# Kernel tuning notes

Measured on AMD Instinct MI355X. Metric: run time of the kernel, lower is better.

Reference implementation:

```python
import jax, jax.numpy as jnp
import numpy as np

H, N, N_SSM, CHANNELS, SEQ_L = 1024, 64, 1024, 1, 2048


def setup_inputs() -> dict:
    key = jax.random.key(0)
    ks = jax.random.split(key, 7)
    log_dt = jax.random.uniform(ks[0], (H,), jnp.float32,
                                minval=np.log(1e-3).astype(np.float32),
                                maxval=np.log(1e-1).astype(np.float32))
    return {
        "L": SEQ_L,
        "log_dt": log_dt,
        "C_re": jax.random.normal(ks[1], (CHANNELS, H, N), jnp.float32),
        "C_im": jax.random.normal(ks[2], (CHANNELS, H, N), jnp.float32),
        "B_re": jax.random.normal(ks[3], (N_SSM, N), jnp.float32),
        "B_im": jax.random.normal(ks[4], (N_SSM, N), jnp.float32),
        "inv_A_real": jax.random.normal(ks[5], (N_SSM, N), jnp.float32),
        "A_imag": jax.random.normal(ks[6], (N_SSM, N), jnp.float32),
    }


def reference(L, log_dt, C_re, C_im, B_re, B_im, inv_A_real, A_imag):
    dt = jnp.exp(log_dt)                                  # (H,)
    C = C_re + 1j * C_im                                  # (channels, H, N)
    A = -jnp.exp(inv_A_real) + 1j * A_imag                # (n_ssm, N)
    B = B_re + 1j * B_im                                  # (n_ssm, N)
    rep = log_dt.shape[0] // A.shape[0]                   # H // n_ssm
    A = jnp.tile(A, (rep, 1))                             # 't n -> (v t) n'
    B = jnp.tile(B, (rep, 1))[None]                       # (1, H, N)
    dtA = A * dt[:, None]                                 # (H, N)
    # C <- (B * C) scaled by bilinear-discretization factor dt / (1 - dtA/2)
    Cm = (B[:, None, :, :] * C).reshape(-1, dt.shape[0], A.shape[-1])  # (channels, H, N)
    Cm = Cm * (dt[:, None] / (1.0 - dtA / 2))             # (channels, H, N)
    # log_vandermonde: K = 2 * Re[ sum_n Cm * exp(dtA * l) ]  -> (channels, H, L)
    l = jnp.arange(L, dtype=jnp.float32)
    vand = jnp.exp(dtA[:, :, None] * l)                   # (H, N, L) complex
    K = 2.0 * jnp.einsum('chn,hnl->chl', Cm, vand).real   # (channels, H, L)
    return K
```

## Files before the change

kernel.cpp:

```cpp
#include <hip/hip_runtime.h>


typedef __attribute__((ext_vector_type(8))) _Float16 f16x8;
typedef __attribute__((ext_vector_type(2))) __fp16   h16x2;
typedef __attribute__((ext_vector_type(4))) float    f32x4;

#define Hdim 1024
#define Ndim 64
#define Ldim 2048
#define KPAD 136
#define CPAD 36

#define LOG2E  1.4426950408889634f
#define INV2PI 0.15915494309189535f

__device__ __forceinline__ void cmul(float& xr, float& xi, float yr, float yi) {
    const float tr = fmaf(xr, yr, -(xi * yi));
    xi = fmaf(xr, yi, xi * yr);
    xr = tr;
}

__device__ __forceinline__ void expz(float ar2, float airev, float t,
                                     float& zr, float& zi) {
    const float e = __builtin_amdgcn_exp2f(ar2 * t);
    float f = airev * t;
    f -= floorf(f);
    zr = e * __builtin_amdgcn_cosf(f);
    zi = e * __builtin_amdgcn_sinf(f);
}

__global__ __launch_bounds__(512, 8) void icmf_mfma(
    const float* __restrict__ log_dt,
    const float* __restrict__ C_re, const float* __restrict__ C_im,
    const float* __restrict__ B_re, const float* __restrict__ B_im,
    const float* __restrict__ inv_A_real, const float* __restrict__ A_imag,
    float* __restrict__ out)
{
    __shared__ __align__(16) _Float16 sA[64][KPAD];
    __shared__ __align__(16) _Float16 sB[32][KPAD];
    __shared__ __align__(16) float    sC[64][CPAD];

    const int h   = blockIdx.x;
    const int tid = threadIdx.x;
    const int w   = tid >> 6;
    const int n   = tid & 63;

    {
        const int idx = h * Ndim + n;
        const float dt = __builtin_amdgcn_exp2f(log_dt[h] * LOG2E);
        const float ar = -dt * __builtin_amdgcn_exp2f(inv_A_real[idx] * LOG2E);
        const float ai =  dt * A_imag[idx];
        const float dre = 1.0f - 0.5f * ar;
        const float dim = -0.5f * ai;
        const float kk  = dt / (dre * dre + dim * dim);
        const float sre =  dre * kk;
        const float sim = -dim * kk;
        const float br = B_re[idx], bi = B_im[idx];
        const float cr = C_re[idx], ci = C_im[idx];
        const float bcr = br * cr - bi * ci;
        const float bci = br * ci + bi * cr;
        const float cmr = 2.0f * (bcr * sre - bci * sim);
        const float cmi = 2.0f * (bcr * sim + bci * sre);
        const float ar2   = ar * LOG2E;
        const float airev = ai * INV2PI;

        float z1r, z1i, z32r, z32i, vr, vi, tr_, ti_;
        expz(ar2, airev, 1.0f,              z1r,  z1i);
        expz(ar2, airev, 32.0f,             z32r, z32i);
        expz(ar2, airev, (float)(4 * w),    vr,   vi);
        expz(ar2, airev, (float)(256 * w),  tr_,  ti_);
        float ur = fmaf(cmr, tr_, -(cmi * ti_));
        float ui = fmaf(cmr, ti_,   cmi * tr_);

#pragma unroll
        for (int s = 0; s < 8; ++s) {
            *(h16x2*)&sA[8 * w + s][2 * n] = __builtin_amdgcn_cvt_pkrtz(ur, -ui);
            cmul(ur, ui, z32r, z32i);
        }
#pragma unroll
        for (int s = 0; s < 4; ++s) {
            *(h16x2*)&sB[4 * w + s][2 * n] = __builtin_amdgcn_cvt_pkrtz(vr, vi);
            cmul(vr, vi, z1r, z1i);
        }
    }
    __syncthreads();

    const int mt   = w >> 1;
    const int nt   = w & 1;
    const int mrow = n & 15;
    const int kgrp = n >> 4;
    f32x4 acc = {0.f, 0.f, 0.f, 0.f};
#pragma unroll
    for (int ks = 0; ks < 4; ++ks) {
        const int k0 = ks * 32 + kgrp * 8;
        const f16x8 af = *(const f16x8*)&sA[16 * mt + mrow][k0];
        const f16x8 bf = *(const f16x8*)&sB[16 * nt + mrow][k0];
        acc = __builtin_amdgcn_mfma_f32_16x16x32_f16(af, bf, acc, 0, 0, 0);
    }

#pragma unroll
    for (int r = 0; r < 4; ++r)
        sC[16 * mt + kgrp * 4 + r][16 * nt + mrow] = acc[r];
    __syncthreads();

    {
        const f32x4 v = *(const f32x4*)&sC[tid >> 3][(tid & 7) * 4];
        *(f32x4*)(out + h * Ldim + tid * 4) = v;
    }
}

extern "C" void kernel_launch(void* const* d_in, const int* in_sizes, int n_in,
                              void* d_out, int out_size, void* d_ws, size_t ws_size,
                              hipStream_t stream) {
    const float* log_dt     = (const float*)d_in[1];
    const float* C_re       = (const float*)d_in[2];
    const float* C_im       = (const float*)d_in[3];
    const float* B_re       = (const float*)d_in[4];
    const float* B_im       = (const float*)d_in[5];
    const float* inv_A_real = (const float*)d_in[6];
    const float* A_imag     = (const float*)d_in[7];
    float* out = (float*)d_out;

    icmf_mfma<<<Hdim, 512, 0, stream>>>(log_dt, C_re, C_im, B_re, B_im,
                                        inv_A_real, A_imag, out);
}
```

Before: 10.54 us.

## Split each head into eight single-wave blocks, dropping barriers and LDS staging

Each head's 64x32 output tile is now computed by eight independent 64-thread blocks instead of one 512-thread block, so no __syncthreads is needed and results go straight from the MFMA accumulator to global memory instead of through an LDS transpose. The cost is redundant work: every block recomputes the per-n discretization parameters and four complex exponentials, and builds 16 rows each of A and B instead of 8 and 4. The direct stores are 64-byte row segments rather than fully coalesced float4 writes, and the launch bounds and block count change to match.

```diff
diff --git a/kernel.cpp b/kernel.cpp
--- a/kernel.cpp
+++ b/kernel.cpp
@@ -9,7 +9,6 @@
 #define Ndim 64
 #define Ldim 2048
 #define KPAD 136
-#define CPAD 36
 
 #define LOG2E  1.4426950408889634f
 #define INV2PI 0.15915494309189535f
@@ -29,21 +28,22 @@
     zi = e * __builtin_amdgcn_sinf(f);
 }
 
-__global__ __launch_bounds__(512, 8) void icmf_mfma(
+__global__ __launch_bounds__(64, 4) void icmf_mfma(
     const float* __restrict__ log_dt,
     const float* __restrict__ C_re, const float* __restrict__ C_im,
     const float* __restrict__ B_re, const float* __restrict__ B_im,
     const float* __restrict__ inv_A_real, const float* __restrict__ A_imag,
     float* __restrict__ out)
 {
-    __shared__ __align__(16) _Float16 sA[64][KPAD];
-    __shared__ __align__(16) _Float16 sB[32][KPAD];
-    __shared__ __align__(16) float    sC[64][CPAD];
+    __shared__ __align__(16) _Float16 sA[16][KPAD];
+    __shared__ __align__(16) _Float16 sB[16][KPAD];
 
-    const int h   = blockIdx.x;
-    const int tid = threadIdx.x;
-    const int w   = tid >> 6;
-    const int n   = tid & 63;
+    const int bid  = blockIdx.x;
+    const int h    = bid >> 3;
+    const int tile = bid & 7;
+    const int mt   = tile >> 1;
+    const int nt   = tile & 1;
+    const int n    = threadIdx.x;
 
     {
         const int idx = h * Ndim + n;
@@ -65,48 +65,40 @@
         const float airev = ai * INV2PI;
 
         float z1r, z1i, z32r, z32i, vr, vi, tr_, ti_;
-        expz(ar2, airev, 1.0f,              z1r,  z1i);
-        expz(ar2, airev, 32.0f,             z32r, z32i);
-        expz(ar2, airev, (float)(4 * w),    vr,   vi);
-        expz(ar2, airev, (float)(256 * w),  tr_,  ti_);
+        expz(ar2, airev, 1.0f,               z1r,  z1i);
+        expz(ar2, airev, 32.0f,              z32r, z32i);
+        expz(ar2, airev, (float)(16 * nt),   vr,   vi);
+        expz(ar2, airev, (float)(512 * mt),  tr_,  ti_);
         float ur = fmaf(cmr, tr_, -(cmi * ti_));
         float ui = fmaf(cmr, ti_,   cmi * tr_);
 
 #pragma unroll
-        for (int s = 0; s < 8; ++s) {
-            *(h16x2*)&sA[8 * w + s][2 * n] = __builtin_amdgcn_cvt_pkrtz(ur, -ui);
+        for (int s = 0; s < 16; ++s) {
+            *(h16x2*)&sA[s][2 * n] = __builtin_amdgcn_cvt_pkrtz(ur, -ui);
             cmul(ur, ui, z32r, z32i);
         }
 #pragma unroll
-        for (int s = 0; s < 4; ++s) {
-            *(h16x2*)&sB[4 * w + s][2 * n] = __builtin_amdgcn_cvt_pkrtz(vr, vi);
+        for (int s = 0; s < 16; ++s) {
+            *(h16x2*)&sB[s][2 * n] = __builtin_amdgcn_cvt_pkrtz(vr, vi);
             cmul(vr, vi, z1r, z1i);
         }
     }
-    __syncthreads();
 
-    const int mt   = w >> 1;
-    const int nt   = w & 1;
     const int mrow = n & 15;
     const int kgrp = n >> 4;
     f32x4 acc = {0.f, 0.f, 0.f, 0.f};
 #pragma unroll
     for (int ks = 0; ks < 4; ++ks) {
         const int k0 = ks * 32 + kgrp * 8;
-        const f16x8 af = *(const f16x8*)&sA[16 * mt + mrow][k0];
-        const f16x8 bf = *(const f16x8*)&sB[16 * nt + mrow][k0];
+        const f16x8 af = *(const f16x8*)&sA[mrow][k0];
+        const f16x8 bf = *(const f16x8*)&sB[mrow][k0];
         acc = __builtin_amdgcn_mfma_f32_16x16x32_f16(af, bf, acc, 0, 0, 0);
     }
 
+    float* o = out + h * Ldim + (16 * mt) * 32 + 16 * nt;
 #pragma unroll
     for (int r = 0; r < 4; ++r)
-        sC[16 * mt + kgrp * 4 + r][16 * nt + mrow] = acc[r];
-    __syncthreads();
-
-    {
-        const f32x4 v = *(const f32x4*)&sC[tid >> 3][(tid & 7) * 4];
-        *(f32x4*)(out + h * Ldim + tid * 4) = v;
-    }
+        o[(kgrp * 4 + r) * 32 + mrow] = acc[r];
 }
 
 extern "C" void kernel_launch(void* const* d_in, const int* in_sizes, int n_in,
@@ -121,6 +113,6 @@
     const float* A_imag     = (const float*)d_in[7];
     float* out = (float*)d_out;
 
-    icmf_mfma<<<Hdim, 512, 0, stream>>>(log_dt, C_re, C_im, B_re, B_im,
-                                        inv_A_real, A_imag, out);
+    icmf_mfma<<<Hdim * 8, 64, 0, stream>>>(log_dt, C_re, C_im, B_re, B_im,
+                                           inv_A_real, A_imag, out);
 }
```

Result: slower. 10.97 us (+4.1%).
